# Optimization experiments

Measured on AMD Instinct MI355X. Metric: run time of the kernel, lower is better.

The kernel has to match this reference:

```python
import jax, jax.numpy as jnp
import numpy as np

VOCAB = 50257
EMB = 512


def setup_inputs() -> dict:
    key = jax.random.key(0)
    k1, k2, k3 = jax.random.split(key, 3)
    input_token_ids = jax.random.randint(k1, (8, 4096), 0, VOCAB, dtype=jnp.int64 if jax.config.jax_enable_x64 else jnp.int32)
    W = jax.random.normal(k2, (EMB, VOCAB), dtype=jnp.float32)  # nn.Linear(vocab, emb).weight
    b = jax.random.normal(k3, (EMB,), dtype=jnp.float32)        # nn.Linear bias
    return {"input_token_ids": input_token_ids, "W": W, "b": b}


def reference(input_token_ids, W, b):
    # one_hot(ids, V) @ W.T + b  ==  W.T[ids] + b   (exact same math, gather form)
    scale = jnp.asarray(EMB, W.dtype) ** 0.5
    emb = jnp.take(W.T, input_token_ids, axis=0)  # [B, S, EMB]
    return (emb + b) * scale
```

## Files before the change

### kernel.cpp

```cpp
#include <hip/hip_runtime.h>


constexpr int VOCAB = 50257;
constexpr int EMB   = 512;
constexpr int NTOK  = 8 * 4096;
constexpr float SCALE = 22.62741699796952f;

constexpr int VB   = 64;
constexpr int NB   = (VOCAB + VB - 1) / VB;
constexpr int CAP  = 96;
constexpr int ESPL = 4;
constexpr int RWV  = 32;
constexpr int RS   = VB + 1;


__global__ __launch_bounds__(256) void build_buckets(
    const int* __restrict__ ids,
    int* __restrict__ counts,
    int* __restrict__ olist,
    int* __restrict__ buckets)
{
    int t = blockIdx.x * 256 + threadIdx.x;
    int id = ids[t];
    int bkt = id >> 6;
    int slot = atomicAdd(&counts[bkt], 1);
    if (slot < CAP) {
        buckets[bkt * CAP + slot] = (t << 6) | (id & 63);
    } else {
        int o = atomicAdd(&counts[NB], 1);
        olist[o] = t;
    }
}

__global__ __launch_bounds__(256) void scatter_main(
    const float* __restrict__ W,
    const float* __restrict__ bias,
    const int*   __restrict__ counts,
    const int*   __restrict__ buckets,
    const int*   __restrict__ olist,
    const int*   __restrict__ ids,
    float*       __restrict__ out)
{
    __shared__ float tile[4][RWV * RS];
    __shared__ int   toks[CAP];
    __shared__ int   s_cnt;

    const int bid  = blockIdx.x;
    const int b    = bid >> 2;
    const int z    = bid & 3;
    const int tid  = threadIdx.x;
    const int lane = tid & 63;
    const int w    = tid >> 6;

    if (tid == 0) s_cnt = counts[b];
    if (tid < CAP) toks[tid] = buckets[b * CAP + tid];
    __syncthreads();
    const int cnt = min(s_cnt, CAP);

    const int e0 = z * 128 + w * RWV;
    const int el = lane & 31;
    const float be = bias[e0 + el];

    const int v = b * VB + lane;
    const float* wsrc = W + (v < VOCAB ? v : VOCAB - 1);

    if (cnt > 0) {
        #pragma unroll
        for (int r = 0; r < RWV; ++r) {
            const float* gp = wsrc + (size_t)(e0 + r) * VOCAB;
            float* lp = &tile[w][r * RS];
            __builtin_amdgcn_global_load_lds(
                (const __attribute__((address_space(1))) void*)gp,
                (__attribute__((address_space(3))) void*)lp, 4, 0, 0);
        }
        asm volatile("s_waitcnt vmcnt(0)" ::: "memory");

        const int half = lane >> 5;
        const float* tw = &tile[w][el * RS];
        for (int i = 0; i < cnt; i += 2) {
            int j  = i + half;
            int jj = j < cnt ? j : cnt - 1;
            int pk = toks[jj];
            int t  = pk >> 6;
            int vl = pk & 63;
            float val = (tw[vl] + be) * SCALE;
            if (j < cnt) out[(size_t)t * EMB + e0 + el] = val;
        }
    }

    if (b == 0) {
        int n = counts[NB];
        for (int ww = w; ww < n; ww += 4) {
            int t  = olist[ww];
            int id = ids[t];
            #pragma unroll
            for (int m = 0; m < 2; ++m) {
                int e = z * 128 + lane + m * 64;
                out[(size_t)t * EMB + e] = (W[(size_t)e * VOCAB + id] + bias[e]) * SCALE;
            }
        }
    }
}

__global__ __launch_bounds__(256) void embed_gather(
    const int*   __restrict__ ids,
    const float* __restrict__ W,
    const float* __restrict__ b,
    float*       __restrict__ out)
{
    int idx4 = blockIdx.x * blockDim.x + threadIdx.x;
    int t    = idx4 >> 7;
    int e    = (idx4 & 127) << 2;
    int id = ids[t];
    float4 bb = *reinterpret_cast<const float4*>(b + e);
    const float* wcol = W + (size_t)id;
    float4 o;
    o.x = (wcol[(size_t)(e + 0) * VOCAB] + bb.x) * SCALE;
    o.y = (wcol[(size_t)(e + 1) * VOCAB] + bb.y) * SCALE;
    o.z = (wcol[(size_t)(e + 2) * VOCAB] + bb.z) * SCALE;
    o.w = (wcol[(size_t)(e + 3) * VOCAB] + bb.w) * SCALE;
    *reinterpret_cast<float4*>(out + (size_t)idx4 * 4) = o;
}

extern "C" void kernel_launch(void* const* d_in, const int* in_sizes, int n_in,
                              void* d_out, int out_size, void* d_ws, size_t ws_size,
                              hipStream_t stream)
{
    const int*   ids  = (const int*)  d_in[0];
    const float* W    = (const float*)d_in[1];
    const float* bias = (const float*)d_in[2];
    float*       out  = (float*)d_out;

    const size_t ws_ints_needed = (size_t)NB + 1 + NTOK + (size_t)NB * CAP;

    if (ws_size >= ws_ints_needed * sizeof(int)) {
        int* counts  = (int*)d_ws;
        int* olist   = counts + NB + 1;
        int* buckets = olist + NTOK;

        hipMemsetAsync(counts, 0, (NB + 1) * sizeof(int), stream);
        build_buckets<<<NTOK / 256, 256, 0, stream>>>(ids, counts, olist, buckets);
        scatter_main<<<NB * ESPL, 256, 0, stream>>>(W, bias, counts, buckets,
                                                    olist, ids, out);
    } else {
        constexpr int total4 = NTOK * EMB / 4;
        embed_gather<<<total4 / 256, 256, 0, stream>>>(ids, W, bias, out);
    }
}
```

Baseline: 195.9 us.

## Restructure scatter kernel with swizzled LDS tile and float4 row writes

The scatter kernel moves from 4 E-chunks of 128 with 256 threads to 2 chunks of 256 with 512 threads. It stages a 256x64 W tile in LDS using an XOR-free rotation swizzle to avoid bank conflicts. Each wave now writes one whole token row segment per iteration with float4 stores, instead of scalar 32-wide stores. Token indices are held in registers and broadcast with readlane rather than staged through shared memory. The cnt>0 early skip is dropped, so every block loads its tile, and the larger 64KB LDS footprint may limit occupancy.

```diff
diff --git a/kernel.cpp b/kernel.cpp
--- a/kernel.cpp
+++ b/kernel.cpp
@@ -9,9 +9,7 @@
 constexpr int VB   = 64;
 constexpr int NB   = (VOCAB + VB - 1) / VB;
 constexpr int CAP  = 96;
-constexpr int ESPL = 4;
-constexpr int RWV  = 32;
-constexpr int RS   = VB + 1;
+constexpr int ECH  = 256;
 
 
 __global__ __launch_bounds__(256) void build_buckets(
@@ -32,7 +30,7 @@
     }
 }
 
-__global__ __launch_bounds__(256) void scatter_main(
+__global__ __launch_bounds__(512) void scatter_main(
     const float* __restrict__ W,
     const float* __restrict__ bias,
     const int*   __restrict__ counts,
@@ -41,61 +39,62 @@
     const int*   __restrict__ ids,
     float*       __restrict__ out)
 {
-    __shared__ float tile[4][RWV * RS];
-    __shared__ int   toks[CAP];
-    __shared__ int   s_cnt;
+    __shared__ float tile[ECH * VB];
 
     const int bid  = blockIdx.x;
-    const int b    = bid >> 2;
-    const int z    = bid & 3;
+    const int b    = bid >> 1;
+    const int z    = bid & 1;
     const int tid  = threadIdx.x;
     const int lane = tid & 63;
     const int w    = tid >> 6;
 
-    if (tid == 0) s_cnt = counts[b];
-    if (tid < CAP) toks[tid] = buckets[b * CAP + tid];
+    const int e0     = z * ECH;
+    const int vstart = min(b * VB, VOCAB - VB);
+    const int vadj   = b * VB - vstart;
+
+    const int cnt   = min(counts[b], CAP);
+    const int tok_a = buckets[b * CAP + lane];
+    const int tok_b = buckets[b * CAP + 64 + (lane & 31)];
+    const float4 b4 = *reinterpret_cast<const float4*>(bias + e0 + 4 * lane);
+
+    #pragma unroll
+    for (int p = 0; p < 32; ++p) {
+        const int r = w * 32 + p;
+        const int srccol = (lane - (r >> 2)) & 63;
+        const float* gp = W + (size_t)(e0 + r) * VOCAB + (vstart + srccol);
+        float* lp = &tile[r * VB];
+        __builtin_amdgcn_global_load_lds(
+            (const __attribute__((address_space(1))) void*)gp,
+            (__attribute__((address_space(3))) void*)lp, 4, 0, 0);
+    }
     __syncthreads();
-    const int cnt = min(s_cnt, CAP);
 
-    const int e0 = z * 128 + w * RWV;
-    const int el = lane & 31;
-    const float be = bias[e0 + el];
-
-    const int v = b * VB + lane;
-    const float* wsrc = W + (v < VOCAB ? v : VOCAB - 1);
-
-    if (cnt > 0) {
-        #pragma unroll
-        for (int r = 0; r < RWV; ++r) {
-            const float* gp = wsrc + (size_t)(e0 + r) * VOCAB;
-            float* lp = &tile[w][r * RS];
-            __builtin_amdgcn_global_load_lds(
-                (const __attribute__((address_space(1))) void*)gp,
-                (__attribute__((address_space(3))) void*)lp, 4, 0, 0);
-        }
-        asm volatile("s_waitcnt vmcnt(0)" ::: "memory");
-
-        const int half = lane >> 5;
-        const float* tw = &tile[w][el * RS];
-        for (int i = 0; i < cnt; i += 2) {
-            int j  = i + half;
-            int jj = j < cnt ? j : cnt - 1;
-            int pk = toks[jj];
-            int t  = pk >> 6;
-            int vl = pk & 63;
-            float val = (tw[vl] + be) * SCALE;
-            if (j < cnt) out[(size_t)t * EMB + e0 + el] = val;
-        }
+    for (int i = w; i < cnt; i += 8) {
+        const int pk = (i < 64) ? __builtin_amdgcn_readlane(tok_a, i)
+                                : __builtin_amdgcn_readlane(tok_b, i - 64);
+        const int t  = pk >> 6;
+        const int vl = (pk & 63) + vadj;
+        const int s  = (vl + lane) & 63;
+        float4 o;
+        o.x = tile[(4 * lane + 0) * VB + s];
+        o.y = tile[(4 * lane + 1) * VB + s];
+        o.z = tile[(4 * lane + 2) * VB + s];
+        o.w = tile[(4 * lane + 3) * VB + s];
+        o.x = (o.x + b4.x) * SCALE;
+        o.y = (o.y + b4.y) * SCALE;
+        o.z = (o.z + b4.z) * SCALE;
+        o.w = (o.w + b4.w) * SCALE;
+        *reinterpret_cast<float4*>(out + (size_t)t * EMB + e0 + 4 * lane) = o;
     }
 
     if (b == 0) {
         int n = counts[NB];
-        for (int ww = w; ww < n; ww += 4) {
+        for (int ww = w; ww < n; ww += 8) {
             int t  = olist[ww];
             int id = ids[t];
             #pragma unroll
-            for (int m = 0; m < 2; ++m) {
-                int e = z * 128 + lane + m * 64;
+            for (int m = 0; m < 4; ++m) {
+                int e = e0 + lane + m * 64;
                 out[(size_t)t * EMB + e] = (W[(size_t)e * VOCAB + id] + bias[e]) * SCALE;
             }
         }
@@ -140,8 +139,8 @@
 
         hipMemsetAsync(counts, 0, (NB + 1) * sizeof(int), stream);
         build_buckets<<<NTOK / 256, 256, 0, stream>>>(ids, counts, olist, buckets);
-        scatter_main<<<NB * ESPL, 256, 0, stream>>>(W, bias, counts, buckets,
-                                                    olist, ids, out);
+        scatter_main<<<NB * 2, 512, 0, stream>>>(W, bias, counts, buckets,
+                                                 olist, ids, out);
     } else {
         constexpr int total4 = NTOK * EMB / 4;
         embed_gather<<<total4 / 256, 256, 0, stream>>>(ids, W, bias, out);
```

New measurement: 195.0 us. About the same (-0.5%).
